# Performance work log

Measured on AMD Instinct MI355X. Metric: run time of the kernel, lower is better.

The kernel has to match this reference:

```python
import jax, jax.numpy as jnp
import numpy as np

ACT_BITS = 8
W_BITS = 8
BN_EPS = 1e-5


def _round_ste(x):
    # straight-through round (HAWQ-style ste_round)
    return x + jax.lax.stop_gradient(jnp.round(x) - x)


def _quant_sym(x, bits):
    # symmetric per-tensor fake quantization; scale treated as constant (EMA min/max in original)
    n = float(2 ** (bits - 1) - 1)
    s = jax.lax.stop_gradient(jnp.maximum(jnp.max(jnp.abs(x)) / n, 1e-8))
    xq = jnp.clip(_round_ste(x / s), -n - 1.0, n) * s
    return xq, s


def _conv(x, w, stride, pad):
    return jax.lax.conv_general_dilated(
        x, w, (stride, stride), [(pad, pad), (pad, pad)],
        dimension_numbers=("NCHW", "OIHW", "NCHW"))


def _quant_bn(x, gamma, beta, mean, var):
    # fold BN into a per-channel scale+bias; quantize the folded scale like a weight
    ws = gamma * jax.lax.rsqrt(var + BN_EPS)          # [C]
    wq, ws_scale = _quant_sym(ws, W_BITS)
    b = beta - mean * wq                               # [C]
    return x * wq[None, :, None, None] + b[None, :, None, None], ws_scale


def setup_inputs() -> dict:
    key = jax.random.key(0)
    ks = jax.random.split(key, 16)
    d = {}
    d["x"] = jax.random.normal(ks[0], (32, 128, 56, 56), jnp.float32)
    d["w1"] = jax.random.normal(ks[1], (256, 128, 3, 3), jnp.float32) * 0.05
    d["w2"] = jax.random.normal(ks[2], (256, 256, 3, 3), jnp.float32) * 0.05
    d["w_id"] = jax.random.normal(ks[3], (256, 128, 1, 1), jnp.float32) * 0.05
    for i, pfx in enumerate(["bn1", "bn2", "id"]):
        k4 = jax.random.split(ks[4 + i], 4)
        d[pfx + "_gamma"] = jax.random.uniform(k4[0], (256,), jnp.float32) + 0.5
        d[pfx + "_beta"] = jax.random.normal(k4[1], (256,), jnp.float32) * 0.1
        d[pfx + "_mean"] = jax.random.normal(k4[2], (256,), jnp.float32) * 0.1
        d[pfx + "_var"] = jax.random.uniform(k4[3], (256,), jnp.float32) + 0.5
    return d


def reference(x, w1, w2, w_id,
              bn1_gamma, bn1_beta, bn1_mean, bn1_var,
              bn2_gamma, bn2_beta, bn2_mean, bn2_var,
              id_gamma, id_beta, id_mean, id_var):
    # quant_act on block input
    xq, act_s = _quant_sym(x, ACT_BITS)

    # identity branch: 1x1 stride-2 quantized conv -> quant_act -> folded quant bn
    w_id_q, _ = _quant_sym(w_id, W_BITS)
    identity = _conv(xq, w_id_q, 2, 0)
    identity, _ = _quant_sym(identity, ACT_BITS)
    identity, _ = _quant_bn(identity, id_gamma, id_beta, id_mean, id_var)

    # main branch conv1 (3x3 stride 2) -> act quant -> bn -> relu -> act quant
    w1_q, _ = _quant_sym(w1, W_BITS)
    h = _conv(xq, w1_q, 2, 1)
    h, _ = _quant_sym(h, ACT_BITS)
    h, _ = _quant_bn(h, bn1_gamma, bn1_beta, bn1_mean, bn1_var)
    h = jax.nn.relu(h)
    h, _ = _quant_sym(h, ACT_BITS)

    # conv2 (3x3 stride 1) -> act quant -> bn
    w2_q, _ = _quant_sym(w2, W_BITS)
    h = _conv(h, w2_q, 1, 1)
    h, _ = _quant_sym(h, ACT_BITS)
    h, _ = _quant_bn(h, bn2_gamma, bn2_beta, bn2_mean, bn2_var)

    # residual add -> int32 requant -> relu
    h = h + identity
    h, out_s = _quant_sym(h, ACT_BITS)
    h = jax.nn.relu(h)
    return h, out_s
```

## Files before the change

kernel.cpp:

```cpp
#include <hip/hip_runtime.h>
#include <limits.h>

#define THREADS 256

typedef int vi4 __attribute__((ext_vector_type(4)));

__device__ __forceinline__ float clamp8f(float q) { return fminf(fmaxf(q, -128.0f), 127.0f); }
__device__ __forceinline__ float sc_from_bits(unsigned b) {
  return fmaxf(__uint_as_float(b) / 127.0f, 1e-8f);
}
__device__ __forceinline__ signed char q8(float v, float s) {
  return (signed char)(int)clamp8f(rintf(v / s));
}


__device__ __forceinline__ void amax_body(const float4* __restrict__ p, int n4, int bid,
                                          int nblocks, int* __restrict__ slot) {
  const int tid = threadIdx.x;
  const int stride = nblocks * THREADS;
  float m = 0.0f;
  int i = bid * THREADS + tid;
  for (; i + 3 * stride < n4; i += 4 * stride) {
    float4 v0 = p[i];
    float4 v1 = p[i + stride];
    float4 v2 = p[i + 2 * stride];
    float4 v3 = p[i + 3 * stride];
    float m0 = fmaxf(fmaxf(fabsf(v0.x), fabsf(v0.y)), fmaxf(fabsf(v0.z), fabsf(v0.w)));
    float m1 = fmaxf(fmaxf(fabsf(v1.x), fabsf(v1.y)), fmaxf(fabsf(v1.z), fabsf(v1.w)));
    float m2 = fmaxf(fmaxf(fabsf(v2.x), fabsf(v2.y)), fmaxf(fabsf(v2.z), fabsf(v2.w)));
    float m3 = fmaxf(fmaxf(fabsf(v3.x), fabsf(v3.y)), fmaxf(fabsf(v3.z), fabsf(v3.w)));
    m = fmaxf(m, fmaxf(fmaxf(m0, m1), fmaxf(m2, m3)));
  }
  for (; i < n4; i += stride) {
    float4 v = p[i];
    m = fmaxf(m, fmaxf(fmaxf(fabsf(v.x), fabsf(v.y)), fmaxf(fabsf(v.z), fabsf(v.w))));
  }
#pragma unroll
  for (int k = 32; k >= 1; k >>= 1) m = fmaxf(m, __shfl_xor(m, k));
  __shared__ float wred[4];
  if ((tid & 63) == 0) wred[tid >> 6] = m;
  __syncthreads();
  if (tid == 0) {
    m = fmaxf(fmaxf(wred[0], wred[1]), fmaxf(wred[2], wred[3]));
    atomicMax(slot, __float_as_int(m));
  }
}

__global__ __launch_bounds__(THREADS) void k_pre(
    int* IS, const float* g1, const float* be1, const float* m1, const float* v1, float* wq1,
    float* b1, const float* g2, const float* be2, const float* m2, const float* v2, float* wq2,
    float* b2, const float* gi, const float* bei, const float* mi, const float* vvi, float* wqi,
    float* bi, const float4* w1, const float4* w2, const float4* wid, const float4* x) {
  int b = blockIdx.x;
  int c = threadIdx.x;
  if (b < 3) {
    const float *gamma, *beta, *mean, *var;
    float *wq, *bb;
    if (b == 0) { gamma = g1; beta = be1; mean = m1; var = v1; wq = wq1; bb = b1; }
    else if (b == 1) { gamma = g2; beta = be2; mean = m2; var = v2; wq = wq2; bb = b2; }
    else { gamma = gi; beta = bei; mean = mi; var = vvi; wq = wqi; bb = bi; }
    __shared__ float red[THREADS];
    float ws = gamma[c] * (1.0f / sqrtf(var[c] + 1e-5f));
    red[c] = fabsf(ws);
    __syncthreads();
    for (int s = THREADS / 2; s > 0; s >>= 1) {
      if (c < s) red[c] = fmaxf(red[c], red[c + s]);
      __syncthreads();
    }
    float sws = fmaxf(red[0] / 127.0f, 1e-8f);
    float q = clamp8f(rintf(ws / sws)) * sws;
    wq[c] = q;
    bb[c] = beta[c] - mean[c] * q;
    return;
  }
  b -= 3;
  if (b < 64) { amax_body(w1, 73728, b, 64, IS + 1); return; }
  b -= 64;
  if (b < 128) { amax_body(w2, 147456, b, 128, IS + 2); return; }
  b -= 128;
  if (b < 16) { amax_body(wid, 8192, b, 16, IS + 3); return; }
  b -= 16;
  amax_body(x, 3211264, b, 512, IS + 0);
}

__global__ __launch_bounds__(THREADS) void k_quant(const float* __restrict__ x,
                                                   int* __restrict__ X8,
                                                   const float* __restrict__ w1f,
                                                   vi4* __restrict__ W1m,
                                                   const float* __restrict__ w2f,
                                                   vi4* __restrict__ W2m,
                                                   const float* __restrict__ widf,
                                                   vi4* __restrict__ Widm,
                                                   const unsigned* __restrict__ ISu) {
  __shared__ signed char tile[56 * 132];
  int b = blockIdx.x;
  int t = threadIdx.x;
  if (b < 1792) {
    float s = sc_from_bits(ISu[0]);
    int h = b % 56, n = b / 56;
    const float* xp = x + ((n * 128) * 56 + h) * 56;
#pragma unroll
    for (int k = 0; k < 28; ++k) {
      int i = t + k * 256;
      int w = i % 56, c = i / 56;
      tile[w * 132 + c] = q8(xp[c * 3136 + w], s);
    }
    __syncthreads();
    int* op = X8 + (n * 56 + h) * 56 * 32;
#pragma unroll
    for (int k = 0; k < 7; ++k) {
      int i = t + k * 256;
      int w = i >> 5, c4 = (i & 31) * 4;
      const signed char* tp = tile + w * 132 + c4;
      op[i] = (int)(unsigned char)tp[0] | ((int)(unsigned char)tp[1] << 8) |
              ((int)(unsigned char)tp[2] << 16) | ((int)(unsigned char)tp[3] << 24);
    }
    return;
  }
  if (b < 1864) {
    int tt = (b - 1792) * THREADS + t;
    float s = sc_from_bits(ISu[1]);
    int lane = tt & 63;
    int cotile = (tt >> 6) & 15;
    int ks = tt >> 10;
    int tap = ks >> 1, kc = ks & 1;
    int kh = tap / 3, kw = tap % 3;
    int co = cotile * 16 + (lane & 15);
    int ci0 = kc * 64 + (lane >> 4) * 16;
    const float* src = w1f + (co * 128 + ci0) * 9 + kh * 3 + kw;
    int r[4];
#pragma unroll
    for (int q = 0; q < 4; ++q) {
      unsigned b0 = (unsigned char)q8(src[(q * 4 + 0) * 9], s);
      unsigned b1 = (unsigned char)q8(src[(q * 4 + 1) * 9], s);
      unsigned b2 = (unsigned char)q8(src[(q * 4 + 2) * 9], s);
      unsigned b3 = (unsigned char)q8(src[(q * 4 + 3) * 9], s);
      r[q] = (int)(b0 | (b1 << 8) | (b2 << 16) | (b3 << 24));
    }
    vi4 v = {r[0], r[1], r[2], r[3]};
    W1m[tt] = v;
    return;
  }
  if (b < 2008) {
    int tt = (b - 1864) * THREADS + t;
    float s = sc_from_bits(ISu[2]);
    int lane = tt & 63;
    int cotile = (tt >> 6) & 15;
    int ks = tt >> 10;
    int tap = ks >> 2, kc = ks & 3;
    int kh = tap / 3, kw = tap % 3;
    int co = cotile * 16 + (lane & 15);
    int ci0 = kc * 64 + (lane >> 4) * 16;
    const float* src = w2f + (co * 256 + ci0) * 9 + kh * 3 + kw;
    int r[4];
#pragma unroll
    for (int q = 0; q < 4; ++q) {
      unsigned b0 = (unsigned char)q8(src[(q * 4 + 0) * 9], s);
      unsigned b1 = (unsigned char)q8(src[(q * 4 + 1) * 9], s);
      unsigned b2 = (unsigned char)q8(src[(q * 4 + 2) * 9], s);
      unsigned b3 = (unsigned char)q8(src[(q * 4 + 3) * 9], s);
      r[q] = (int)(b0 | (b1 << 8) | (b2 << 16) | (b3 << 24));
    }
    vi4 v = {r[0], r[1], r[2], r[3]};
    W2m[tt] = v;
    return;
  }
  {
    int tt = (b - 2008) * THREADS + t;
    float s = sc_from_bits(ISu[3]);
    int lane = tt & 63;
    int cotile = (tt >> 6) & 15;
    int ks = tt >> 10;
    int co = cotile * 16 + (lane & 15);
    int ci0 = ks * 64 + (lane >> 4) * 16;
    const float* src = widf + co * 128 + ci0;
    int r[4];
#pragma unroll
    for (int q = 0; q < 4; ++q) {
      unsigned b0 = (unsigned char)q8(src[q * 4 + 0], s);
      unsigned b1 = (unsigned char)q8(src[q * 4 + 1], s);
      unsigned b2 = (unsigned char)q8(src[q * 4 + 2], s);
      unsigned b3 = (unsigned char)q8(src[q * 4 + 3], s);
      r[q] = (int)(b0 | (b1 << 8) | (b2 << 16) | (b3 << 24));
    }
    vi4 v = {r[0], r[1], r[2], r[3]};
    Widm[tt] = v;
  }
}

#define MFMA_I8(a, b, c) __builtin_amdgcn_mfma_i32_16x16x64_i8(a, b, c, 0, 0, 0)

__global__ __launch_bounds__(THREADS, 3) void k_conv1(const int* __restrict__ X8,
                                                      const vi4* __restrict__ W1m,
                                                      const vi4* __restrict__ Widm,
                                                      int* __restrict__ H1, int* __restrict__ IDI,
                                                      int* __restrict__ maxS,
                                                      int* __restrict__ minS,
                                                      int* __restrict__ maxabs_id) {
  __shared__ __align__(16) int lds[5 * 58 * 36];
  __shared__ int sMax[2][128], sMin[2][128], redA[4];
  const int tid = threadIdx.x;
  const int bx = blockIdx.x;
  const int n = bx / 28, rr = bx % 28;
  const int hp = rr >> 1, nh = rr & 1;
  const int ho0 = hp * 2;
  vi4 zero = {0, 0, 0, 0};

  for (int r = 0; r < 5; ++r) {
    int h = 2 * ho0 - 1 + r;
    int* dst = lds + r * 58 * 36;
    if (h >= 0 && h < 56) {
      const vi4* src = (const vi4*)(X8 + (n * 56 + h) * 56 * 32);
      for (int i4 = tid; i4 < 448; i4 += THREADS) {
        int col = i4 >> 3, c = (i4 & 7) * 4;
        *(vi4*)(dst + (col + 1) * 36 + c) = src[i4];
      }
      if (tid < 32) dst[tid] = 0;
      else if (tid >= 128 && tid < 160) dst[57 * 36 + (tid - 128)] = 0;
    } else {
      for (int i4 = tid; i4 < 522; i4 += THREADS) ((vi4*)dst)[i4] = zero;
    }
  }
  __syncthreads();

  const int lane = tid & 63, wv = tid >> 6;
  const int mw = wv & 1, nw = wv >> 1;
  const int lm = lane & 15, quad = lane >> 4;
  const int woc0 = lm, woc1 = (16 + lm) > 27 ? 27 : (16 + lm);
  const int choff = quad * 4;
  const int ho = ho0 + mw;
  const int obase = ((n * 28 + ho) * 28) * 256;
  const int ctbase = nh * 8 + nw * 4;

  vi4 acc[2][4];
  vi4 bA[4], bB[4];
  vi4 a0A, a1A, a0B, a1B;

#pragma unroll
  for (int mt = 0; mt < 2; ++mt)
#pragma unroll
    for (int ct = 0; ct < 4; ++ct) acc[mt][ct] = zero;
  const vi4* wibase = Widm + ctbase * 64 + lane;
  {
    const int ro = (2 * mw + 1) * 58;
#pragma unroll
    for (int kc = 0; kc < 2; ++kc) {
      vi4 a0 = *(const vi4*)(lds + (ro + 2 * woc0 + 1) * 36 + kc * 16 + choff);
      vi4 a1 = *(const vi4*)(lds + (ro + 2 * woc1 + 1) * 36 + kc * 16 + choff);
#pragma unroll
      for (int ct = 0; ct < 4; ++ct) {
        vi4 b = wibase[kc * 1024 + ct * 64];
        acc[0][ct] = MFMA_I8(a0, b, acc[0][ct]);
        acc[1][ct] = MFMA_I8(a1, b, acc[1][ct]);
      }
    }
  }
  int am = 0;
#pragma unroll
  for (int ct = 0; ct < 4; ++ct) {
    const int co = (ctbase + ct) * 16 + lm;
#pragma unroll
    for (int mt = 0; mt < 2; ++mt)
#pragma unroll
      for (int r = 0; r < 4; ++r) {
        int wo = mt * 16 + quad * 4 + r;
        if (wo < 28) {
          int v = acc[mt][ct][r];
          IDI[obase + wo * 256 + co] = v;
          am = max(am, v < 0 ? -v : v);
        }
      }
  }
#pragma unroll
  for (int k = 32; k >= 1; k >>= 1) am = max(am, __shfl_xor(am, k));
  if (lane == 0) redA[wv] = am;

#pragma unroll
  for (int mt = 0; mt < 2; ++mt)
#pragma unroll
    for (int ct = 0; ct < 4; ++ct) acc[mt][ct] = zero;
  const vi4* wbase = W1m + ctbase * 64 + lane;
#pragma unroll
  for (int ct = 0; ct < 4; ++ct) bA[ct] = wbase[ct * 64];
  {
    const int ro = (2 * mw) * 58;
    a0A = *(const vi4*)(lds + (ro + 2 * woc0) * 36 + choff);
    a1A = *(const vi4*)(lds + (ro + 2 * woc1) * 36 + choff);
  }
#pragma unroll 1
  for (int ks = 0; ks < 18; ks += 2) {
    {
      const int ksn = ks + 1;
      const int khn = (ksn >= 6) + (ksn >= 12);
      const int t2 = ksn - khn * 6;
      const int kwn = t2 >> 1, kcn = t2 & 1;
#pragma unroll
      for (int ct = 0; ct < 4; ++ct) bB[ct] = wbase[ksn * 1024 + ct * 64];
      const int ro = (2 * mw + khn) * 58;
      a0B = *(const vi4*)(lds + (ro + 2 * woc0 + kwn) * 36 + kcn * 16 + choff);
      a1B = *(const vi4*)(lds + (ro + 2 * woc1 + kwn) * 36 + kcn * 16 + choff);
    }
#pragma unroll
    for (int ct = 0; ct < 4; ++ct) {
      acc[0][ct] = MFMA_I8(a0A, bA[ct], acc[0][ct]);
      acc[1][ct] = MFMA_I8(a1A, bA[ct], acc[1][ct]);
    }
    if (ks + 2 < 18) {
      const int ksn = ks + 2;
      const int khn = (ksn >= 6) + (ksn >= 12);
      const int t2 = ksn - khn * 6;
      const int kwn = t2 >> 1, kcn = t2 & 1;
#pragma unroll
      for (int ct = 0; ct < 4; ++ct) bA[ct] = wbase[ksn * 1024 + ct * 64];
      const int ro = (2 * mw + khn) * 58;
      a0A = *(const vi4*)(lds + (ro + 2 * woc0 + kwn) * 36 + kcn * 16 + choff);
      a1A = *(const vi4*)(lds + (ro + 2 * woc1 + kwn) * 36 + kcn * 16 + choff);
    }
#pragma unroll
    for (int ct = 0; ct < 4; ++ct) {
      acc[0][ct] = MFMA_I8(a0B, bB[ct], acc[0][ct]);
      acc[1][ct] = MFMA_I8(a1B, bB[ct], acc[1][ct]);
    }
  }

#pragma unroll
  for (int ct = 0; ct < 4; ++ct) {
    const int co = (ctbase + ct) * 16 + lm;
    int vmax = INT_MIN, vmin = INT_MAX;
#pragma unroll
    for (int mt = 0; mt < 2; ++mt)
#pragma unroll
      for (int r = 0; r < 4; ++r) {
        int wo = mt * 16 + quad * 4 + r;
        if (wo < 28) {
          int v = acc[mt][ct][r];
          H1[obase + wo * 256 + co] = v;
          vmax = max(vmax, v);
          vmin = min(vmin, v);
        }
      }
    vmax = max(vmax, __shfl_xor(vmax, 16));
    vmax = max(vmax, __shfl_xor(vmax, 32));
    vmin = min(vmin, __shfl_xor(vmin, 16));
    vmin = min(vmin, __shfl_xor(vmin, 32));
    if (lane < 16) {
      sMax[mw][nw * 64 + ct * 16 + lane] = vmax;
      sMin[mw][nw * 64 + ct * 16 + lane] = vmin;
    }
  }
  __syncthreads();
  if (tid < 128) {
    int row = n * 14 + hp;
    maxS[row * 256 + nh * 128 + tid] = max(sMax[0][tid], sMax[1][tid]);
    minS[row * 256 + nh * 128 + tid] = min(sMin[0][tid], sMin[1][tid]);
  }
  if (tid == 0) {
    int a = max(max(redA[0], redA[1]), max(redA[2], redA[3]));
    atomicMax(maxabs_id, a);
  }
}

__global__ __launch_bounds__(1024) void k_rs1(int* __restrict__ IS, float* __restrict__ SC,
                                              const int* __restrict__ maxS,
                                              const int* __restrict__ minS,
                                              const float* __restrict__ wq1,
                                              const float* __restrict__ b1) {
  __shared__ int pMax[4][256], pMin[4][256];
  __shared__ int ri[256];
  __shared__ float rf[256];
  int t = threadIdx.x;
  int c = t & 255, part = t >> 8;
  int vmax = INT_MIN, vmin = INT_MAX;
#pragma unroll 4
  for (int r = part; r < 448; r += 4) {
    vmax = max(vmax, maxS[r * 256 + c]);
    vmin = min(vmin, minS[r * 256 + c]);
  }
  pMax[part][c] = vmax;
  pMin[part][c] = vmin;
  __syncthreads();
  if (t < 256) {
    vmax = max(max(pMax[0][c], pMax[1][c]), max(pMax[2][c], pMax[3][c]));
    vmin = min(min(pMin[0][c], pMin[1][c]), min(pMin[2][c], pMin[3][c]));
    int a1 = vmax < 0 ? -vmax : vmax;
    int a0 = vmin < 0 ? -vmin : vmin;
    ri[c] = max(a1, a0);
  }
  __syncthreads();
  for (int s = 128; s > 0; s >>= 1) {
    if (t < s) ri[t] = max(ri[t], ri[t + s]);
    __syncthreads();
  }
  int mh1 = ri[0];
  const unsigned* ISu = (const unsigned*)IS;
  float sx = sc_from_bits(ISu[0]);
  float sw1 = sc_from_bits(ISu[1]);
  float sxw = sx * sw1;
  float s_h1 = fmaxf(sxw * (float)mh1 / 127.0f, 1e-8f);
  if (t < 256) {
    float wq = wq1[c], bbc = b1[c];
    float q1 = clamp8f(rintf((float)vmax * sxw / s_h1));
    float q0 = clamp8f(rintf((float)vmin * sxw / s_h1));
    float hv1 = q1 * s_h1, hv0 = q0 * s_h1;
    float y1 = fmaxf(hv1 * wq + bbc, 0.0f);
    float y0 = fmaxf(hv0 * wq + bbc, 0.0f);
    rf[c] = fmaxf(y1, y0);
  }
  __syncthreads();
  for (int s = 128; s > 0; s >>= 1) {
    if (t < s) rf[t] = fmaxf(rf[t], rf[t + s]);
    __syncthreads();
  }
  if (t == 0) {
    IS[4] = mh1;
    SC[7] = rf[0];
    SC[8] = s_h1;
    SC[9] = fmaxf(rf[0] / 127.0f, 1e-8f);
    float swid = sc_from_bits(ISu[3]);
    SC[10] = fmaxf(sx * swid * (float)IS[5] / 127.0f, 1e-8f);
  }
}

__device__ __forceinline__ signed char qact(int v, float sxw, float s_h1, float s_y2, float wq,
                                            float bb) {
  float hf = (float)v * sxw;
  float q = clamp8f(rintf(hf / s_h1));
  float hv = q * s_h1;
  float y = fmaxf(hv * wq + bb, 0.0f);
  float a = fminf(fmaxf(rintf(y / s_y2), -128.0f), 127.0f);
  return (signed char)(int)a;
}

__global__ __launch_bounds__(THREADS) void k_qh1(const int4* __restrict__ H1,
                                                 char4* __restrict__ A2,
                                                 const float* __restrict__ SC,
                                                 const float* __restrict__ wq1,
                                                 const float* __restrict__ b1) {
  int t = blockIdx.x * THREADS + threadIdx.x;
  const unsigned* ISu = (const unsigned*)SC;
  float sx = sc_from_bits(ISu[0]);
  float sw1 = sc_from_bits(ISu[1]);
  float sxw = sx * sw1;
  float s_h1 = SC[8];
  float s_y2 = SC[9];
  int4 v = H1[t];
  int c0 = (t * 4) & 255;
  char4 r;
  r.x = qact(v.x, sxw, s_h1, s_y2, wq1[c0], b1[c0]);
  r.y = qact(v.y, sxw, s_h1, s_y2, wq1[c0 + 1], b1[c0 + 1]);
  r.z = qact(v.z, sxw, s_h1, s_y2, wq1[c0 + 2], b1[c0 + 2]);
  r.w = qact(v.w, sxw, s_h1, s_y2, wq1[c0 + 3], b1[c0 + 3]);
  A2[t] = r;
}

__global__ __launch_bounds__(THREADS, 4) void k_conv2(const int* __restrict__ A2,
                                                      const vi4* __restrict__ W2m,
                                                      int* __restrict__ H2,
                                                      int* __restrict__ maxabs_h2) {
  __shared__ __align__(16) int lds[4 * 30 * 68];
  __shared__ int redA[4];
  const int tid = threadIdx.x;
  const int bx = blockIdx.x;
  const int n = bx / 28, rr = bx % 28;
  const int hp = rr >> 1, nh = rr & 1;
  const int ho0 = hp * 2;
  vi4 zero = {0, 0, 0, 0};

  for (int r = 0; r < 4; ++r) {
    int h = ho0 - 1 + r;
    int* dst = lds + r * 30 * 68;
    if (h >= 0 && h < 28) {
      const vi4* src = (const vi4*)(A2 + (n * 28 + h) * 28 * 64);
      for (int i4 = tid; i4 < 448; i4 += THREADS) {
        int col = i4 >> 4, c = (i4 & 15) * 4;
        *(vi4*)(dst + (col + 1) * 68 + c) = src[i4];
      }
      if (tid < 64) dst[tid] = 0;
      else if (tid >= 128 && tid < 192) dst[29 * 68 + (tid - 128)] = 0;
    } else {
      for (int i4 = tid; i4 < 510; i4 += THREADS) ((vi4*)dst)[i4] = zero;
    }
  }
  __syncthreads();

  const int lane = tid & 63, wv = tid >> 6;
  const int mw = wv & 1, nw = wv >> 1;
  const int lm = lane & 15, quad = lane >> 4;
  const int woc0 = lm, woc1 = (16 + lm) > 27 ? 27 : (16 + lm);
  const int choff = quad * 4;
  const int ho = ho0 + mw;
  const int ctbase = nh * 8 + nw * 4;

  vi4 acc[2][4];
  vi4 bA[4], bB[4];
  vi4 a0A, a1A, a0B, a1B;
#pragma unroll
  for (int mt = 0; mt < 2; ++mt)
#pragma unroll
    for (int ct = 0; ct < 4; ++ct) acc[mt][ct] = zero;

  const vi4* wbase = W2m + ctbase * 64 + lane;
#pragma unroll
  for (int ct = 0; ct < 4; ++ct) bA[ct] = wbase[ct * 64];
  {
    const int ro = mw * 30;
    a0A = *(const vi4*)(lds + (ro + woc0) * 68 + choff);
    a1A = *(const vi4*)(lds + (ro + woc1) * 68 + choff);
  }
#pragma unroll 1
  for (int ks = 0; ks < 36; ks += 2) {
    {
      const int ksn = ks + 1;
      const int khn = (ksn >= 12) + (ksn >= 24);
      const int t2 = ksn - khn * 12;
      const int kwn = t2 >> 2, kcn = t2 & 3;
#pragma unroll
      for (int ct = 0; ct < 4; ++ct) bB[ct] = wbase[ksn * 1024 + ct * 64];
      const int ro = (mw + khn) * 30;
      a0B = *(const vi4*)(lds + (ro + woc0 + kwn) * 68 + kcn * 16 + choff);
      a1B = *(const vi4*)(lds + (ro + woc1 + kwn) * 68 + kcn * 16 + choff);
    }
#pragma unroll
    for (int ct = 0; ct < 4; ++ct) {
      acc[0][ct] = MFMA_I8(a0A, bA[ct], acc[0][ct]);
      acc[1][ct] = MFMA_I8(a1A, bA[ct], acc[1][ct]);
    }
    if (ks + 2 < 36) {
      const int ksn = ks + 2;
      const int khn = (ksn >= 12) + (ksn >= 24);
      const int t2 = ksn - khn * 12;
      const int kwn = t2 >> 2, kcn = t2 & 3;
#pragma unroll
      for (int ct = 0; ct < 4; ++ct) bA[ct] = wbase[ksn * 1024 + ct * 64];
      const int ro = (mw + khn) * 30;
      a0A = *(const vi4*)(lds + (ro + woc0 + kwn) * 68 + kcn * 16 + choff);
      a1A = *(const vi4*)(lds + (ro + woc1 + kwn) * 68 + kcn * 16 + choff);
    }
#pragma unroll
    for (int ct = 0; ct < 4; ++ct) {
      acc[0][ct] = MFMA_I8(a0B, bB[ct], acc[0][ct]);
      acc[1][ct] = MFMA_I8(a1B, bB[ct], acc[1][ct]);
    }
  }

  const int obase = ((n * 28 + ho) * 28) * 256;
  int am = 0;
#pragma unroll
  for (int ct = 0; ct < 4; ++ct) {
    const int co = (ctbase + ct) * 16 + lm;
#pragma unroll
    for (int mt = 0; mt < 2; ++mt)
#pragma unroll
      for (int r = 0; r < 4; ++r) {
        int wo = mt * 16 + quad * 4 + r;
        if (wo < 28) {
          int v = acc[mt][ct][r];
          H2[obase + wo * 256 + co] = v;
          am = max(am, v < 0 ? -v : v);
        }
      }
  }
#pragma unroll
  for (int k = 32; k >= 1; k >>= 1) am = max(am, __shfl_xor(am, k));
  if (lane == 0) redA[wv] = am;
  __syncthreads();
  if (tid == 0) {
    int a = max(max(redA[0], redA[1]), max(redA[2], redA[3]));
    atomicMax(maxabs_h2, a);
  }
}

struct SumParams {
  float sxw2, s_h2, sxwid, s_idq;
};
__device__ __forceinline__ float sum_val(int v2, int vi, const SumParams& P, float wq2c, float b2c,
                                         float wqidc, float bidc) {
  float q2 = clamp8f(rintf((float)v2 * P.sxw2 / P.s_h2));
  float z = (q2 * P.s_h2) * wq2c + b2c;
  float qi = clamp8f(rintf((float)vi * P.sxwid / P.s_idq));
  float zi = (qi * P.s_idq) * wqidc + bidc;
  return z + zi;
}
__device__ __forceinline__ SumParams make_params(const float* SC, const int* IS) {
  const unsigned* ISu = (const unsigned*)IS;
  SumParams P;
  float sx = sc_from_bits(ISu[0]);
  float sw2 = sc_from_bits(ISu[2]);
  float swid = sc_from_bits(ISu[3]);
  float s_y2 = SC[9];
  P.s_idq = SC[10];
  P.sxw2 = s_y2 * sw2;
  P.s_h2 = fmaxf(P.sxw2 * (float)IS[6] / 127.0f, 1e-8f);
  P.sxwid = sx * swid;
  return P;
}

__global__ __launch_bounds__(THREADS) void k_absmax2(const int4* __restrict__ H2,
                                                     const int4* __restrict__ IDI,
                                                     const float* __restrict__ SC,
                                                     const int* __restrict__ IS,
                                                     const float* __restrict__ wq2,
                                                     const float* __restrict__ b2,
                                                     const float* __restrict__ wqid,
                                                     const float* __restrict__ bidp,
                                                     int* __restrict__ slot) {
  __shared__ float pw2[256], pb2[256], pwi[256], pbi[256];
  int tid = threadIdx.x;
  pw2[tid] = wq2[tid];
  pb2[tid] = b2[tid];
  pwi[tid] = wqid[tid];
  pbi[tid] = bidp[tid];
  __syncthreads();
  SumParams P = make_params(SC, IS);
  const int n4 = 1605632;
  const int stride = gridDim.x * THREADS;
  float m = 0.0f;
  for (int i = blockIdx.x * THREADS + tid; i < n4; i += stride) {
    int4 v2 = H2[i];
    int4 vi = IDI[i];
    int c0 = (i * 4) & 255;
    m = fmaxf(m, fabsf(sum_val(v2.x, vi.x, P, pw2[c0], pb2[c0], pwi[c0], pbi[c0])));
    m = fmaxf(m, fabsf(sum_val(v2.y, vi.y, P, pw2[c0 + 1], pb2[c0 + 1], pwi[c0 + 1], pbi[c0 + 1])));
    m = fmaxf(m, fabsf(sum_val(v2.z, vi.z, P, pw2[c0 + 2], pb2[c0 + 2], pwi[c0 + 2], pbi[c0 + 2])));
    m = fmaxf(m, fabsf(sum_val(v2.w, vi.w, P, pw2[c0 + 3], pb2[c0 + 3], pwi[c0 + 3], pbi[c0 + 3])));
  }
#pragma unroll
  for (int k = 32; k >= 1; k >>= 1) m = fmaxf(m, __shfl_xor(m, k));
  __shared__ float wred[4];
  if ((tid & 63) == 0) wred[tid >> 6] = m;
  __syncthreads();
  if (tid == 0) {
    m = fmaxf(fmaxf(wred[0], wred[1]), fmaxf(wred[2], wred[3]));
    atomicMax(slot, __float_as_int(m));
  }
}

__global__ __launch_bounds__(THREADS) void k_out(const int* __restrict__ H2,
                                                 const int* __restrict__ IDI,
                                                 const float* __restrict__ SC,
                                                 const int* __restrict__ IS,
                                                 const float* __restrict__ wq2,
                                                 const float* __restrict__ b2,
                                                 const float* __restrict__ wqid,
                                                 const float* __restrict__ bidp,
                                                 float* __restrict__ out) {
  __shared__ float tile[64 * 57];
  __shared__ float pw2[64], pb2[64], pwi[64], pbi[64];
  int tid = threadIdx.x;
  int b = blockIdx.x;
  int ct = b & 3;
  int rt = (b >> 2) % 14;
  int n = b / 56;
  int c0 = ct * 64;
  int r0 = rt * 56;
  if (tid < 64) {
    pw2[tid] = wq2[c0 + tid];
    pb2[tid] = b2[c0 + tid];
    pwi[tid] = wqid[c0 + tid];
    pbi[tid] = bidp[c0 + tid];
  }
  __syncthreads();
  SumParams P = make_params(SC, IS);
  float out_s = fmaxf(__uint_as_float(((const unsigned*)IS)[11]) / 127.0f, 1e-8f);

  const int base = (n * 784 + r0) * 256 + c0;
#pragma unroll
  for (int k = 0; k < 14; ++k) {
    int idx = tid + k * 256;
    int rl = idx >> 6;
    int cl = idx & 63;
    int e = base + rl * 256 + cl;
    float sv = sum_val(H2[e], IDI[e], P, pw2[cl], pb2[cl], pwi[cl], pbi[cl]);
    float q = clamp8f(rintf(sv / out_s));
    tile[cl * 57 + rl] = q > 0.0f ? q * out_s : 0.0f;
  }
  __syncthreads();
  float* ob = out + n * 200704 + c0 * 784 + r0;
#pragma unroll
  for (int k = 0; k < 14; ++k) {
    int idx = tid + k * 256;
    int cl = idx / 56;
    int rl = idx % 56;
    ob[cl * 784 + rl] = tile[cl * 57 + rl];
  }
  if (b == 0 && tid == 0) out[6422528] = out_s;
}

extern "C" void kernel_launch(void* const* d_in, const int* in_sizes, int n_in, void* d_out,
                              int out_size, void* d_ws, size_t ws_size, hipStream_t stream) {
  (void)in_sizes; (void)n_in; (void)out_size; (void)ws_size;
  const float* x = (const float*)d_in[0];
  const float* w1 = (const float*)d_in[1];
  const float* w2 = (const float*)d_in[2];
  const float* wid = (const float*)d_in[3];
  const float* bn1g = (const float*)d_in[4];
  const float* bn1b = (const float*)d_in[5];
  const float* bn1m = (const float*)d_in[6];
  const float* bn1v = (const float*)d_in[7];
  const float* bn2g = (const float*)d_in[8];
  const float* bn2b = (const float*)d_in[9];
  const float* bn2m = (const float*)d_in[10];
  const float* bn2v = (const float*)d_in[11];
  const float* idg = (const float*)d_in[12];
  const float* idb = (const float*)d_in[13];
  const float* idm = (const float*)d_in[14];
  const float* idv = (const float*)d_in[15];

  char* ws = (char*)d_ws;
  float* SC = (float*)ws;
  int* IS = (int*)ws;
  unsigned* ISu = (unsigned*)ws;
  float* wq1 = (float*)(ws + 3072);
  float* b1 = (float*)(ws + 4096);
  float* wq2 = (float*)(ws + 5120);
  float* b2 = (float*)(ws + 6144);
  float* wqid = (float*)(ws + 7168);
  float* bid = (float*)(ws + 8192);
  char* X8 = ws + 16384;
  char* A2 = X8;
  char* W1m = X8 + 12845056;
  char* W2m = W1m + 294912;
  char* Widm = W2m + 589824;
  int* H1 = (int*)(Widm + 32768);
  int* H2 = H1;
  int* IDI = (int*)((char*)H1 + 25690112);
  float* out = (float*)d_out;
  int* maxS = (int*)d_out;
  int* minS = maxS + 448 * 256;

  k_pre<<<723, THREADS, 0, stream>>>(IS, bn1g, bn1b, bn1m, bn1v, wq1, b1, bn2g, bn2b, bn2m, bn2v,
                                     wq2, b2, idg, idb, idm, idv, wqid, bid, (const float4*)w1,
                                     (const float4*)w2, (const float4*)wid, (const float4*)x);
  k_quant<<<2016, THREADS, 0, stream>>>(x, (int*)X8, w1, (vi4*)W1m, w2, (vi4*)W2m, wid,
                                        (vi4*)Widm, ISu);
  k_conv1<<<896, THREADS, 0, stream>>>((const int*)X8, (const vi4*)W1m, (const vi4*)Widm, H1, IDI,
                                       maxS, minS, IS + 5);
  k_rs1<<<1, 1024, 0, stream>>>(IS, SC, maxS, minS, wq1, b1);
  k_qh1<<<6272, THREADS, 0, stream>>>((const int4*)H1, (char4*)A2, SC, wq1, b1);
  k_conv2<<<896, THREADS, 0, stream>>>((const int*)A2, (const vi4*)W2m, H2, IS + 6);
  k_absmax2<<<1024, THREADS, 0, stream>>>((const int4*)H2, (const int4*)IDI, SC, IS, wq2, b2, wqid,
                                          bid, IS + 11);
  k_out<<<1792, THREADS, 0, stream>>>(H2, IDI, SC, IS, wq2, b2, wqid, bid, out);
}
```

Baseline: 253.6 us.

## Retile conv1 so each block covers one output row and all 256 channels

Each conv1 block used to handle two output rows and half the output channels, staging five input rows in LDS. It now handles a single output row and all 256 channels across its four waves, staging only three input rows. LDS use drops and launch bounds rise to 4 blocks per CU, and the shared-memory min/max merge is replaced by each wave writing its per-channel partials straight to global memory. In exchange, adjacent output rows now reload the overlapping input row, and twice as many partial rows are written and then reduced by k_rs1.

```diff
diff --git a/kernel.cpp b/kernel.cpp
--- a/kernel.cpp
+++ b/kernel.cpp
@@ -190,24 +190,22 @@
 
 #define MFMA_I8(a, b, c) __builtin_amdgcn_mfma_i32_16x16x64_i8(a, b, c, 0, 0, 0)
 
-__global__ __launch_bounds__(THREADS, 3) void k_conv1(const int* __restrict__ X8,
+__global__ __launch_bounds__(THREADS, 4) void k_conv1(const int* __restrict__ X8,
                                                       const vi4* __restrict__ W1m,
                                                       const vi4* __restrict__ Widm,
                                                       int* __restrict__ H1, int* __restrict__ IDI,
                                                       int* __restrict__ maxS,
                                                       int* __restrict__ minS,
                                                       int* __restrict__ maxabs_id) {
-  __shared__ __align__(16) int lds[5 * 58 * 36];
-  __shared__ int sMax[2][128], sMin[2][128], redA[4];
+  __shared__ __align__(16) int lds[3 * 58 * 36];
+  __shared__ int redA[4];
   const int tid = threadIdx.x;
   const int bx = blockIdx.x;
-  const int n = bx / 28, rr = bx % 28;
-  const int hp = rr >> 1, nh = rr & 1;
-  const int ho0 = hp * 2;
+  const int n = bx / 28, ho = bx % 28;
   vi4 zero = {0, 0, 0, 0};
 
-  for (int r = 0; r < 5; ++r) {
-    int h = 2 * ho0 - 1 + r;
+  for (int r = 0; r < 3; ++r) {
+    int h = 2 * ho - 1 + r;
     int* dst = lds + r * 58 * 36;
     if (h >= 0 && h < 56) {
       const vi4* src = (const vi4*)(X8 + (n * 56 + h) * 56 * 32);
@@ -223,14 +221,12 @@
   }
   __syncthreads();
 
-  const int lane = tid & 63, wv = tid >> 6;
-  const int mw = wv & 1, nw = wv >> 1;
+  const int lane = tid & 63, nw = tid >> 6;
   const int lm = lane & 15, quad = lane >> 4;
   const int woc0 = lm, woc1 = (16 + lm) > 27 ? 27 : (16 + lm);
   const int choff = quad * 4;
-  const int ho = ho0 + mw;
   const int obase = ((n * 28 + ho) * 28) * 256;
-  const int ctbase = nh * 8 + nw * 4;
+  const int ctbase = nw * 4;
 
   vi4 acc[2][4];
   vi4 bA[4], bB[4];
@@ -242,7 +238,7 @@
     for (int ct = 0; ct < 4; ++ct) acc[mt][ct] = zero;
   const vi4* wibase = Widm + ctbase * 64 + lane;
   {
-    const int ro = (2 * mw + 1) * 58;
+    const int ro = 58;
 #pragma unroll
     for (int kc = 0; kc < 2; ++kc) {
       vi4 a0 = *(const vi4*)(lds + (ro + 2 * woc0 + 1) * 36 + kc * 16 + choff);
@@ -273,7 +269,7 @@
   }
 #pragma unroll
   for (int k = 32; k >= 1; k >>= 1) am = max(am, __shfl_xor(am, k));
-  if (lane == 0) redA[wv] = am;
+  if (lane == 0) redA[nw] = am;
 
 #pragma unroll
   for (int mt = 0; mt < 2; ++mt)
@@ -283,9 +279,8 @@
 #pragma unroll
   for (int ct = 0; ct < 4; ++ct) bA[ct] = wbase[ct * 64];
   {
-    const int ro = (2 * mw) * 58;
-    a0A = *(const vi4*)(lds + (ro + 2 * woc0) * 36 + choff);
-    a1A = *(const vi4*)(lds + (ro + 2 * woc1) * 36 + choff);
+    a0A = *(const vi4*)(lds + (2 * woc0) * 36 + choff);
+    a1A = *(const vi4*)(lds + (2 * woc1) * 36 + choff);
   }
 #pragma unroll 1
   for (int ks = 0; ks < 18; ks += 2) {
@@ -296,7 +291,7 @@
       const int kwn = t2 >> 1, kcn = t2 & 1;
 #pragma unroll
       for (int ct = 0; ct < 4; ++ct) bB[ct] = wbase[ksn * 1024 + ct * 64];
-      const int ro = (2 * mw + khn) * 58;
+      const int ro = khn * 58;
       a0B = *(const vi4*)(lds + (ro + 2 * woc0 + kwn) * 36 + kcn * 16 + choff);
       a1B = *(const vi4*)(lds + (ro + 2 * woc1 + kwn) * 36 + kcn * 16 + choff);
     }
@@ -312,7 +307,7 @@
       const int kwn = t2 >> 1, kcn = t2 & 1;
 #pragma unroll
       for (int ct = 0; ct < 4; ++ct) bA[ct] = wbase[ksn * 1024 + ct * 64];
-      const int ro = (2 * mw + khn) * 58;
+      const int ro = khn * 58;
       a0A = *(const vi4*)(lds + (ro + 2 * woc0 + kwn) * 36 + kcn * 16 + choff);
       a1A = *(const vi4*)(lds + (ro + 2 * woc1 + kwn) * 36 + kcn * 16 + choff);
     }
@@ -323,6 +318,7 @@
     }
   }
 
+  const int row = n * 28 + ho;
 #pragma unroll
   for (int ct = 0; ct < 4; ++ct) {
     const int co = (ctbase + ct) * 16 + lm;
@@ -344,16 +340,11 @@
     vmin = min(vmin, __shfl_xor(vmin, 16));
     vmin = min(vmin, __shfl_xor(vmin, 32));
     if (lane < 16) {
-      sMax[mw][nw * 64 + ct * 16 + lane] = vmax;
-      sMin[mw][nw * 64 + ct * 16 + lane] = vmin;
-    }
-  }
-  __syncthreads();
-  if (tid < 128) {
-    int row = n * 14 + hp;
-    maxS[row * 256 + nh * 128 + tid] = max(sMax[0][tid], sMax[1][tid]);
-    minS[row * 256 + nh * 128 + tid] = min(sMin[0][tid], sMin[1][tid]);
-  }
+      maxS[row * 256 + (ctbase + ct) * 16 + lane] = vmax;
+      minS[row * 256 + (ctbase + ct) * 16 + lane] = vmin;
+    }
+  }
+  __syncthreads();
   if (tid == 0) {
     int a = max(max(redA[0], redA[1]), max(redA[2], redA[3]));
     atomicMax(maxabs_id, a);
@@ -372,7 +363,7 @@
   int c = t & 255, part = t >> 8;
   int vmax = INT_MIN, vmin = INT_MAX;
 #pragma unroll 4
-  for (int r = part; r < 448; r += 4) {
+  for (int r = part; r < 896; r += 4) {
     vmax = max(vmax, maxS[r * 256 + c]);
     vmin = min(vmin, minS[r * 256 + c]);
   }
@@ -726,7 +717,7 @@
   int* IDI = (int*)((char*)H1 + 25690112);
   float* out = (float*)d_out;
   int* maxS = (int*)d_out;
-  int* minS = maxS + 448 * 256;
+  int* minS = maxS + 896 * 256;
 
   k_pre<<<723, THREADS, 0, stream>>>(IS, bn1g, bn1b, bn1m, bn1v, wq1, b1, bn2g, bn2b, bn2m, bn2v,
                                      wq2, b2, idg, idb, idm, idv, wqid, bid, (const float4*)w1,
```

Result: slower. 262.1 us (+3.3%).
